# Performance work log

Hardware: AMD Instinct MI355X
Metric: run time of the kernel (lower is better)

## Reference

```python
import jax, jax.numpy as jnp
import numpy as np

N = 1_000_000   # total elements
G = 100_000     # number of groups (all guaranteed non-empty)
D = 128         # emb_dim


def setup_inputs() -> dict:
    key = jax.random.key(0)
    k1, k2, k3, k4, k5, k6 = jax.random.split(key, 6)
    embeddings = jax.random.normal(k1, (N, D), dtype=jnp.float32)
    # sorted segment ids with every id in [0, G) present at least once
    extra = jax.random.randint(k2, (N - G,), 0, G, dtype=jnp.int32)
    seg_ids = jnp.sort(jnp.concatenate([jnp.arange(G, dtype=jnp.int32), extra]))
    # nn.Linear default init: U(-1/sqrt(fan_in), 1/sqrt(fan_in))
    s = 1.0 / np.sqrt(D)
    Wq = jax.random.uniform(k3, (D, D), jnp.float32, -s, s)
    bq = jax.random.uniform(k4, (D,), jnp.float32, -s, s)
    Wk = jax.random.uniform(k5, (D, D), jnp.float32, -s, s)
    bk = jax.random.uniform(k6, (D,), jnp.float32, -s, s)
    return {"embeddings": embeddings, "seg_ids": seg_ids,
            "Wq": Wq, "bq": bq, "Wk": Wk, "bk": bk}


def reference(embeddings, seg_ids, Wq, bq, Wk, bk):
    # keys = key_layer(embeddings), computed once for all elements  [N, D]
    keys = embeddings @ Wk.T + bk
    # index of the LAST element of each (sorted, contiguous) segment
    counts = jax.ops.segment_sum(jnp.ones_like(seg_ids), seg_ids, num_segments=G)
    last_idx = jnp.cumsum(counts) - 1                       # [G]
    # query = query_layer(group_emb[-1])                    [G, D]
    q = embeddings[last_idx] @ Wq.T + bq
    # per-element attention logit: <q[group(i)], keys[i]>   [N]
    logits = jnp.sum(q[seg_ids] * keys, axis=-1)
    # segment-wise stable softmax
    m = jax.ops.segment_max(logits, seg_ids, num_segments=G)
    e = jnp.exp(logits - m[seg_ids])
    denom = jax.ops.segment_sum(e, seg_ids, num_segments=G)
    w = e / denom[seg_ids]                                  # [N]
    # weighted sum of keys per segment                      [G, D]
    out = jax.ops.segment_sum(w[:, None] * keys, seg_ids, num_segments=G)
    return out
```

## Files before the change

kernel.cpp:

```cpp
#include <hip/hip_runtime.h>
#include <math.h>

typedef _Float16 half8  __attribute__((ext_vector_type(8)));
typedef _Float16 half2v __attribute__((ext_vector_type(2)));
typedef float    floatx4 __attribute__((ext_vector_type(4)));

#define LGKM_FENCE() asm volatile("s_waitcnt lgkmcnt(0)" ::: "memory")

__global__ void seg_bounds_kernel(const int* __restrict__ seg,
                                  int* __restrict__ seg_start, int N, int G) {
    int i = blockIdx.x * 256 + threadIdx.x;
    if (i >= N) return;
    int s = seg[i];
    if (i == 0 || s != seg[i - 1]) seg_start[s] = i;
    if (i == N - 1) seg_start[G] = N;
}

__device__ inline half8 pack8(float4 a, float4 b) {
    half8 r;
    r[0] = (_Float16)a.x; r[1] = (_Float16)a.y; r[2] = (_Float16)a.z; r[3] = (_Float16)a.w;
    r[4] = (_Float16)b.x; r[5] = (_Float16)b.y; r[6] = (_Float16)b.z; r[7] = (_Float16)b.w;
    return r;
}

__global__ __launch_bounds__(64, 2) void fused_attn_kernel(
    const float* __restrict__ emb, const int* __restrict__ seg_start,
    const float* __restrict__ Wq, const float* __restrict__ bq,
    const float* __restrict__ Wk, const float* __restrict__ bk,
    float* __restrict__ out)
{
    __shared__ alignas(16) _Float16 keys_lds[16][136];
    __shared__ alignas(16) _Float16 q_lds[8][136];
    __shared__ alignas(16) float    L_lds[16];

    const int lane = threadIdx.x;
    const int m    = lane & 15;
    const int quad = lane >> 4;

    const int g0 = blockIdx.x * 8;
    const int s0 = seg_start[g0];
    const int e0 = seg_start[g0 + 8];

    int sb[9];
#pragma unroll
    for (int i = 0; i <= 8; ++i) sb[i] = seg_start[g0 + i];

    float bkv[8];
#pragma unroll
    for (int c = 0; c < 8; ++c) bkv[c] = bk[16 * c + m];

    {
        int  qm   = (m < 8) ? m : 7;
        long qrow = (long)seg_start[g0 + qm + 1] - 1;
        half8 aq[4];
#pragma unroll
        for (int kq = 0; kq < 4; ++kq) {
            const float4* p = (const float4*)(emb + qrow * 128 + kq * 32 + quad * 8);
            aq[kq] = pack8(p[0], p[1]);
        }
#pragma unroll
        for (int c = 0; c < 8; ++c) {
            float bqc = bq[16 * c + m];
            floatx4 acc = {bqc, bqc, bqc, bqc};
#pragma unroll
            for (int kq = 0; kq < 4; ++kq) {
                const float4* wp = (const float4*)(Wq + (16 * c + m) * 128 + kq * 32 + quad * 8);
                half8 bf = pack8(wp[0], wp[1]);
                acc = __builtin_amdgcn_mfma_f32_16x16x32_f16(aq[kq], bf, acc, 0, 0, 0);
            }
            if (quad < 2) {
#pragma unroll
                for (int r = 0; r < 4; ++r)
                    q_lds[quad * 4 + r][16 * c + m] = (_Float16)acc[r];
            }
        }
    }
    LGKM_FENCE();

    half8 wkf[8][4];
#pragma unroll
    for (int c = 0; c < 8; ++c)
#pragma unroll
        for (int kq = 0; kq < 4; ++kq) {
            const float4* wp = (const float4*)(Wk + (16 * c + m) * 128 + kq * 32 + quad * 8);
            wkf[c][kq] = pack8(wp[0], wp[1]);
        }

    const int nt = (e0 - s0 + 15) >> 4;

    float4 pre[8];
    {
        long prow = (long)min(s0 + m, e0 - 1);
#pragma unroll
        for (int kq = 0; kq < 4; ++kq) {
            const float4* p = (const float4*)(emb + prow * 128 + kq * 32 + quad * 8);
            pre[2 * kq] = p[0]; pre[2 * kq + 1] = p[1];
        }
    }

    int   g = g0;
    int   cur_end = sb[1];
    float run_m = -INFINITY, run_d = 0.f, acc0 = 0.f, acc1 = 0.f;

    for (int tt = 0; tt < nt; ++tt) {
        const int t   = s0 + tt * 16;
        const int cnt = min(16, e0 - t);

        half8 ak[4];
#pragma unroll
        for (int kq = 0; kq < 4; ++kq)
            ak[kq] = pack8(pre[2 * kq], pre[2 * kq + 1]);

        if (tt + 1 < nt) {
            long nrow = (long)min(t + 16 + m, e0 - 1);
#pragma unroll
            for (int kq = 0; kq < 4; ++kq) {
                const float4* p = (const float4*)(emb + nrow * 128 + kq * 32 + quad * 8);
                pre[2 * kq] = p[0]; pre[2 * kq + 1] = p[1];
            }
        }

#pragma unroll
        for (int c = 0; c < 8; ++c) {
            floatx4 acc = {bkv[c], bkv[c], bkv[c], bkv[c]};
#pragma unroll
            for (int kq = 0; kq < 4; ++kq)
                acc = __builtin_amdgcn_mfma_f32_16x16x32_f16(ak[kq], wkf[c][kq], acc, 0, 0, 0);
#pragma unroll
            for (int r = 0; r < 4; ++r)
                keys_lds[quad * 4 + r][16 * c + m] = (_Float16)acc[r];
        }
        LGKM_FENCE();

        floatx4 lacc = {0.f, 0.f, 0.f, 0.f};
#pragma unroll
        for (int kq = 0; kq < 4; ++kq) {
            half8 af = *(const half8*)&keys_lds[m][kq * 32 + quad * 8];
            half8 bf = *(const half8*)&q_lds[m & 7][kq * 32 + quad * 8];
            lacc = __builtin_amdgcn_mfma_f32_16x16x32_f16(af, bf, lacc, 0, 0, 0);
        }
#pragma unroll
        for (int r = 0; r < 4; ++r) {
            int rowc = min(t + quad * 4 + r, e0 - 1);
            int sl = 0;
#pragma unroll
            for (int i = 1; i < 8; ++i) sl += (rowc >= sb[i]) ? 1 : 0;
            if (m == sl) L_lds[quad * 4 + r] = lacc[r];
        }
        LGKM_FENCE();

        float lg[16];
#pragma unroll
        for (int i = 0; i < 4; ++i) {
            float4 v = *(const float4*)&L_lds[4 * i];
            lg[4 * i] = v.x; lg[4 * i + 1] = v.y; lg[4 * i + 2] = v.z; lg[4 * i + 3] = v.w;
        }
        half2v kv[16];
#pragma unroll
        for (int r = 0; r < 16; ++r)
            kv[r] = *(const half2v*)&keys_lds[r][2 * lane];

#pragma unroll
        for (int rl = 0; rl < 16; ++rl) {
            if (rl < cnt) {
                int row = t + rl;
                while (row >= cur_end) {
                    float inv = 1.0f / run_d;
                    float2 o; o.x = acc0 * inv; o.y = acc1 * inv;
                    *(float2*)(out + (long)g * 128 + 2 * lane) = o;
                    ++g;
                    cur_end = seg_start[g + 1];
                    run_m = -INFINITY; run_d = 0.f; acc0 = 0.f; acc1 = 0.f;
                }
                float logit = lg[rl];
                float k0 = (float)kv[rl][0], k1 = (float)kv[rl][1];
                float nm = fmaxf(run_m, logit);
                float sc = __expf(run_m - nm);
                float e  = __expf(logit - nm);
                run_d = run_d * sc + e;
                acc0  = acc0 * sc + e * k0;
                acc1  = acc1 * sc + e * k1;
                run_m = nm;
            }
        }
    }
    {
        float inv = 1.0f / run_d;
        float2 o; o.x = acc0 * inv; o.y = acc1 * inv;
        *(float2*)(out + (long)g * 128 + 2 * lane) = o;
    }
}

extern "C" void kernel_launch(void* const* d_in, const int* in_sizes, int n_in,
                              void* d_out, int out_size, void* d_ws, size_t ws_size,
                              hipStream_t stream) {
    const float* emb = (const float*)d_in[0];
    const int*   seg = (const int*)d_in[1];
    const float* Wq  = (const float*)d_in[2];
    const float* bq  = (const float*)d_in[3];
    const float* Wk  = (const float*)d_in[4];
    const float* bk  = (const float*)d_in[5];
    float* out = (float*)d_out;

    const int N = in_sizes[1];
    const int G = out_size / 128;

    int* seg_start = (int*)d_ws;

    seg_bounds_kernel<<<(N + 255) / 256, 256, 0, stream>>>(seg, seg_start, N, G);
    fused_attn_kernel<<<G / 8, 64, 0, stream>>>(emb, seg_start, Wq, bq, Wk, bk, out);
}
```

Baseline: 800.3 us.

## Process 16 groups per block with per-tile max-rescaled online softmax

Each wave now handles 16 groups instead of 8, so all four MFMA output quads produce useful query rows and the Wk/Wq fragment loads are amortised over twice as many segments. Segment bounds and per-group running maxima are kept one per lane and exchanged with shuffles, which removes the 8-way comparison chain and the global seg_start reloads. The per-row online softmax rescale (two exps per element) becomes one tile-level max reduction and one exp per element. This halves the grid to G/16 blocks, which reduces the number of waves available to hide memory latency, and makes each block's serial loop longer.

Measured after the change: 872.1 us. 9.0% more time.

```diff
diff --git a/kernel.cpp b/kernel.cpp
--- a/kernel.cpp
+++ b/kernel.cpp
@@ -30,28 +30,25 @@
     float* __restrict__ out)
 {
     __shared__ alignas(16) _Float16 keys_lds[16][136];
-    __shared__ alignas(16) _Float16 q_lds[8][136];
+    __shared__ alignas(16) _Float16 q_lds[16][136];
     __shared__ alignas(16) float    L_lds[16];
 
     const int lane = threadIdx.x;
     const int m    = lane & 15;
     const int quad = lane >> 4;
 
-    const int g0 = blockIdx.x * 8;
-    const int s0 = seg_start[g0];
-    const int e0 = seg_start[g0 + 8];
-
-    int sb[9];
-#pragma unroll
-    for (int i = 0; i <= 8; ++i) sb[i] = seg_start[g0 + i];
+    const int g0 = blockIdx.x * 16;
+    const int lo = seg_start[g0 + m];
+    const int hi = seg_start[g0 + m + 1];
+    const int s0 = __shfl(lo, 0);
+    const int e0 = __shfl(hi, 15);
 
     float bkv[8];
 #pragma unroll
     for (int c = 0; c < 8; ++c) bkv[c] = bk[16 * c + m];
 
     {
-        int  qm   = (m < 8) ? m : 7;
-        long qrow = (long)seg_start[g0 + qm + 1] - 1;
+        long qrow = (long)hi - 1;
         half8 aq[4];
 #pragma unroll
         for (int kq = 0; kq < 4; ++kq) {
@@ -68,14 +65,17 @@
                 half8 bf = pack8(wp[0], wp[1]);
                 acc = __builtin_amdgcn_mfma_f32_16x16x32_f16(aq[kq], bf, acc, 0, 0, 0);
             }
-            if (quad < 2) {
-#pragma unroll
-                for (int r = 0; r < 4; ++r)
-                    q_lds[quad * 4 + r][16 * c + m] = (_Float16)acc[r];
-            }
+#pragma unroll
+            for (int r = 0; r < 4; ++r)
+                q_lds[quad * 4 + r][16 * c + m] = (_Float16)acc[r];
         }
     }
     LGKM_FENCE();
+
+    half8 qf[4];
+#pragma unroll
+    for (int kq = 0; kq < 4; ++kq)
+        qf[kq] = *(const half8*)&q_lds[m][kq * 32 + quad * 8];
 
     half8 wkf[8][4];
 #pragma unroll
@@ -99,8 +99,10 @@
     }
 
     int   g = g0;
-    int   cur_end = sb[1];
-    float run_m = -INFINITY, run_d = 0.f, acc0 = 0.f, acc1 = 0.f;
+    int   cur_end = __shfl(hi, 0);
+    float M_run = -INFINITY;
+    float M_cur = 0.f;
+    float d_acc = 0.f, acc0 = 0.f, acc1 = 0.f;
 
     for (int tt = 0; tt < nt; ++tt) {
         const int t   = s0 + tt * 16;
@@ -136,16 +138,12 @@
 #pragma unroll
         for (int kq = 0; kq < 4; ++kq) {
             half8 af = *(const half8*)&keys_lds[m][kq * 32 + quad * 8];
-            half8 bf = *(const half8*)&q_lds[m & 7][kq * 32 + quad * 8];
-            lacc = __builtin_amdgcn_mfma_f32_16x16x32_f16(af, bf, lacc, 0, 0, 0);
+            lacc = __builtin_amdgcn_mfma_f32_16x16x32_f16(af, qf[kq], lacc, 0, 0, 0);
         }
 #pragma unroll
         for (int r = 0; r < 4; ++r) {
-            int rowc = min(t + quad * 4 + r, e0 - 1);
-            int sl = 0;
-#pragma unroll
-            for (int i = 1; i < 8; ++i) sl += (rowc >= sb[i]) ? 1 : 0;
-            if (m == sl) L_lds[quad * 4 + r] = lacc[r];
+            int rowc = t + quad * 4 + r;
+            if (rowc >= lo && rowc < hi) L_lds[quad * 4 + r] = lacc[r];
         }
         LGKM_FENCE();
 
@@ -159,33 +157,47 @@
 #pragma unroll
         for (int r = 0; r < 16; ++r)
             kv[r] = *(const half2v*)&keys_lds[r][2 * lane];
+
+        float tv[16];
+#pragma unroll
+        for (int r = 0; r < 16; ++r) {
+            int row = t + r;
+            tv[r] = (row >= lo && row < hi) ? lg[r] : -INFINITY;
+        }
+#pragma unroll
+        for (int s = 8; s > 0; s >>= 1)
+#pragma unroll
+            for (int r = 0; r < s; ++r) tv[r] = fmaxf(tv[r], tv[r + s]);
+        float M_new = fmaxf(M_run, tv[0]);
+        float sc = (M_run == -INFINITY) ? 0.f : __expf(M_run - M_new);
+        M_run = M_new;
+
+        float sc_c = __shfl(sc, g - g0);
+        M_cur      = __shfl(M_new, g - g0);
+        acc0 *= sc_c; acc1 *= sc_c; d_acc *= sc_c;
 
 #pragma unroll
         for (int rl = 0; rl < 16; ++rl) {
             if (rl < cnt) {
                 int row = t + rl;
                 while (row >= cur_end) {
-                    float inv = 1.0f / run_d;
+                    float inv = 1.0f / d_acc;
                     float2 o; o.x = acc0 * inv; o.y = acc1 * inv;
                     *(float2*)(out + (long)g * 128 + 2 * lane) = o;
                     ++g;
-                    cur_end = seg_start[g + 1];
-                    run_m = -INFINITY; run_d = 0.f; acc0 = 0.f; acc1 = 0.f;
+                    cur_end = __shfl(hi, g - g0);
+                    M_cur   = __shfl(M_new, g - g0);
+                    acc0 = 0.f; acc1 = 0.f; d_acc = 0.f;
                 }
-                float logit = lg[rl];
-                float k0 = (float)kv[rl][0], k1 = (float)kv[rl][1];
-                float nm = fmaxf(run_m, logit);
-                float sc = __expf(run_m - nm);
-                float e  = __expf(logit - nm);
-                run_d = run_d * sc + e;
-                acc0  = acc0 * sc + e * k0;
-                acc1  = acc1 * sc + e * k1;
-                run_m = nm;
+                float e = __expf(lg[rl] - M_cur);
+                acc0  += e * (float)kv[rl][0];
+                acc1  += e * (float)kv[rl][1];
+                d_acc += e;
             }
         }
     }
     {
-        float inv = 1.0f / run_d;
+        float inv = 1.0f / d_acc;
         float2 o; o.x = acc0 * inv; o.y = acc1 * inv;
         *(float2*)(out + (long)g * 128 + 2 * lane) = o;
     }
@@ -208,5 +220,5 @@
     int* seg_start = (int*)d_ws;
 
     seg_bounds_kernel<<<(N + 255) / 256, 256, 0, stream>>>(seg, seg_start, N, G);
-    fused_attn_kernel<<<G / 8, 64, 0, stream>>>(emb, seg_start, Wq, bq, Wk, bk, out);
-}
+    fused_attn_kernel<<<G / 16, 64, 0, stream>>>(emb, seg_start, Wq, bq, Wk, bk, out);
+}
```
